# Performance work log

Hardware: AMD Instinct MI355X
Metric: run time of the kernel (lower is better)

## Reference

```python
import jax, jax.numpy as jnp
import numpy as np

N_HEAD = 16
CHUNK_SIZE = 64
TOP_B = 8
LOCAL_WINDOW = 256


def _l2_normalize(x, eps=1e-12):
    # matches torch F.normalize(dim=-1): x / max(||x||, eps)
    n = jnp.sqrt(jnp.sum(x * x, axis=-1, keepdims=True))
    return x / jnp.maximum(n, eps)


def setup_inputs() -> dict:
    key = jax.random.key(0)
    ks = jax.random.split(key, 9)
    B, T, C = 2, 2048, 1024
    s = lambda fan_in: 1.0 / np.sqrt(fan_in)
    return {
        "x": jax.random.normal(ks[0], (B, T, C), jnp.float32),
        "Wqkv": jax.random.normal(ks[1], (C, 3 * C), jnp.float32) * s(C),
        "bqkv": jax.random.normal(ks[2], (3 * C,), jnp.float32) * 0.02,
        "Wproj": jax.random.normal(ks[3], (C, C), jnp.float32) * s(C),
        "bproj": jax.random.normal(ks[4], (C,), jnp.float32) * 0.02,
        "Wrouter": jax.random.normal(ks[5], (C, 32), jnp.float32) * s(C),
        "brouter": jax.random.normal(ks[6], (32,), jnp.float32) * 0.02,
        "Wq_rt": jax.random.normal(ks[7], (C, 32), jnp.float32) * s(C),
        "bq_rt": jax.random.normal(ks[8], (32,), jnp.float32) * 0.02,
    }


def reference(x, Wqkv, bqkv, Wproj, bproj, Wrouter, brouter, Wq_rt, bq_rt):
    B, T, C = x.shape
    H = N_HEAD
    D = C // H

    # --- qkv projection ---
    qkv = x @ Wqkv + bqkv                       # [B,T,3C]
    q, k, v = jnp.split(qkv, 3, axis=-1)
    q = q.reshape(B, T, H, D).transpose(0, 2, 1, 3)  # [B,H,T,D]
    k = k.reshape(B, T, H, D).transpose(0, 2, 1, 3)
    v = v.reshape(B, T, H, D).transpose(0, 2, 1, 3)

    # --- routing (T > local_window + chunk_size) ---
    num_chunks = T // CHUNK_SIZE                 # T divisible -> no padding, mask all-True
    chunk_means = x.reshape(B, num_chunks, CHUNK_SIZE, C).mean(axis=2)  # [B,N,C]
    routing_embeds = chunk_means @ Wrouter + brouter                     # [B,N,32]
    q_rt = _l2_normalize(x @ Wq_rt + bq_rt)                              # [B,T,32]
    re_n = _l2_normalize(routing_embeds)
    routing_scores = jnp.einsum('btd,bnd->btn', q_rt, re_n)              # [B,T,N]
    _, chunk_indices = jax.lax.top_k(routing_scores, TOP_B)              # [B,T,top_b]

    # --- dense causal attention (forward path uses is_causal SDPA) ---
    scale = 1.0 / jnp.sqrt(jnp.asarray(D, x.dtype))
    scores = jnp.einsum('bhqd,bhkd->bhqk', q, k) * scale                 # [B,H,T,T]
    causal = jnp.tril(jnp.ones((T, T), dtype=bool))
    scores = jnp.where(causal[None, None], scores, -jnp.inf)
    attn = jax.nn.softmax(scores, axis=-1)
    y = jnp.einsum('bhqk,bhkd->bhqd', attn, v)                           # [B,H,T,D]
    y = y.transpose(0, 2, 1, 3).reshape(B, T, C)
    y = y @ Wproj + bproj

    return y, chunk_indices, routing_scores, routing_embeds
```

## Files before the change

kernel.cpp:

```cpp
#include <hip/hip_runtime.h>
#include <hip/hip_bf16.h>
#include <math.h>

#define B_   2
#define T_   2048
#define C_   1024
#define H_   16
#define D_   64
#define NCH  32
#define RD   32
#define TOPB 8

typedef __attribute__((ext_vector_type(8))) short bf16x8;
typedef __attribute__((ext_vector_type(4))) float f32x4;

static __device__ __forceinline__ unsigned short f2b(float f) {
    return __bfloat16_as_ushort(__float2bfloat16(f));
}

#define SCALE2 0.18033688f

__global__ __launch_bounds__(256) void prep_fused(
    const float* __restrict__ x, unsigned short* __restrict__ xb,
    const float* __restrict__ Wqkv, unsigned short* __restrict__ Wqt,
    const float* __restrict__ Wproj, unsigned short* __restrict__ Wpt,
    const float* __restrict__ Wq_rt, const float* __restrict__ bq_rt,
    float* __restrict__ qrt, float* __restrict__ cm)
{
    __shared__ float smem[64 * 65];
    const int bid = blockIdx.x;
    const int tid = threadIdx.x;

    if (bid < 2048) {
        const int i = bid * 256 + tid;
        float4 a = ((const float4*)x)[i * 2];
        float4 b = ((const float4*)x)[i * 2 + 1];
        bf16x8 o;
        o[0] = (short)f2b(a.x); o[1] = (short)f2b(a.y);
        o[2] = (short)f2b(a.z); o[3] = (short)f2b(a.w);
        o[4] = (short)f2b(b.x); o[5] = (short)f2b(b.y);
        o[6] = (short)f2b(b.z); o[7] = (short)f2b(b.w);
        *(bf16x8*)&xb[(size_t)i * 8] = o;
    } else if (bid < 3072) {
        const float* W; unsigned short* Wt; int N, local;
        if (bid < 2816) { W = Wqkv;  Wt = Wqt; N = 3072; local = bid - 2048; }
        else            { W = Wproj; Wt = Wpt; N = 1024; local = bid - 2816; }
        const int nblk = N >> 6;
        const int n0 = (local % nblk) * 64, k0 = (local / nblk) * 64;
        float (*t)[65] = (float(*)[65])smem;
#pragma unroll
        for (int i = 0; i < 4; i++) {
            const int f = tid + i * 256;
            const int r = f >> 4, c4 = (f & 15) * 4;
            float4 v = *(const float4*)&W[(size_t)(k0 + r) * N + n0 + c4];
            t[r][c4 + 0] = v.x; t[r][c4 + 1] = v.y;
            t[r][c4 + 2] = v.z; t[r][c4 + 3] = v.w;
        }
        __syncthreads();
#pragma unroll
        for (int i = 0; i < 2; i++) {
            const int s = tid + i * 256;
            const int rn = s >> 3, ck8 = (s & 7) * 8;
            bf16x8 o;
#pragma unroll
            for (int j = 0; j < 8; j++) o[j] = (short)f2b(t[ck8 + j][rn]);
            *(bf16x8*)&Wt[(size_t)(n0 + rn) * 1024 + k0 + ck8] = o;
        }
    } else if (bid < 4096) {
        float (*part)[4][32] = (float(*)[4][32])smem;
        const int r0 = (bid - 3072) * 4;
        const int g = tid >> 5;
        const int n = tid & 31;
        const float* w  = Wq_rt + (size_t)(g * 128) * RD + n;
        const float* a0 = x + (size_t)(r0 + 0) * C_ + g * 128;
        const float* a1 = x + (size_t)(r0 + 1) * C_ + g * 128;
        const float* a2 = x + (size_t)(r0 + 2) * C_ + g * 128;
        const float* a3 = x + (size_t)(r0 + 3) * C_ + g * 128;
        float acc0 = 0.f, acc1 = 0.f, acc2 = 0.f, acc3 = 0.f;
#pragma unroll 8
        for (int i = 0; i < 128; i += 4) {
            const float w0 = w[(i + 0) * RD];
            const float w1 = w[(i + 1) * RD];
            const float w2 = w[(i + 2) * RD];
            const float w3 = w[(i + 3) * RD];
            float4 x0 = *(const float4*)&a0[i];
            float4 x1 = *(const float4*)&a1[i];
            float4 x2 = *(const float4*)&a2[i];
            float4 x3 = *(const float4*)&a3[i];
            acc0 += x0.x * w0; acc0 += x0.y * w1; acc0 += x0.z * w2; acc0 += x0.w * w3;
            acc1 += x1.x * w0; acc1 += x1.y * w1; acc1 += x1.z * w2; acc1 += x1.w * w3;
            acc2 += x2.x * w0; acc2 += x2.y * w1; acc2 += x2.z * w2; acc2 += x2.w * w3;
            acc3 += x3.x * w0; acc3 += x3.y * w1; acc3 += x3.z * w2; acc3 += x3.w * w3;
        }
        part[g][0][n] = acc0;
        part[g][1][n] = acc1;
        part[g][2][n] = acc2;
        part[g][3][n] = acc3;
        __syncthreads();
        if (g < 4) {
            float s = part[0][g][n];
#pragma unroll
            for (int gg = 1; gg < 8; gg++) s += part[gg][g][n];
            s += bq_rt[n];
            float ss = s * s;
#pragma unroll
            for (int off = 16; off >= 1; off >>= 1) ss += __shfl_xor(ss, off, 32);
            qrt[(size_t)(r0 + g) * RD + n] = s / fmaxf(sqrtf(ss), 1e-12f);
        }
    } else {
        const int local = bid - 4096;
        const int bc = local & 63;
        const int b = bc >> 5, n = bc & 31;
        const int c = (local >> 6) * 256 + tid;
        const float* xp = x + ((size_t)b * T_ + n * 64) * C_;
        float s = 0.f;
        for (int i = 0; i < 64; i++) s += xp[(size_t)i * C_ + c];
        cm[(size_t)bc * C_ + c] = s * (1.0f / 64.0f);
    }
}

__global__ void embeds_kernel(const float* __restrict__ cm, const float* __restrict__ W,
                              const float* __restrict__ bias,
                              float* __restrict__ emb_out, float* __restrict__ ren)
{
    const int row  = blockIdx.x * 8 + (threadIdx.x >> 5);
    const int lane = threadIdx.x & 31;
    if (row >= B_ * NCH) return;
    const float* a = cm + (size_t)row * C_;
    float acc = 0.f;
    for (int k = 0; k < C_; k += 4) {
        float4 a4 = *(const float4*)&a[k];
        acc += a4.x * W[(k + 0) * RD + lane];
        acc += a4.y * W[(k + 1) * RD + lane];
        acc += a4.z * W[(k + 2) * RD + lane];
        acc += a4.w * W[(k + 3) * RD + lane];
    }
    acc += bias[lane];
    emb_out[(size_t)row * RD + lane] = acc;
    float ss = acc * acc;
#pragma unroll
    for (int off = 16; off >= 1; off >>= 1) ss += __shfl_xor(ss, off, 32);
    ren[(size_t)row * RD + lane] = acc / fmaxf(sqrtf(ss), 1e-12f);
}

__global__ __launch_bounds__(512, 4) void gemm_qkv_128x256(
    const unsigned short* __restrict__ A, const unsigned short* __restrict__ Bt,
    const float* __restrict__ bias,
    unsigned short* __restrict__ qp, unsigned short* __restrict__ kp,
    unsigned short* __restrict__ vp, int M, int N, int K)
{
    __shared__ unsigned short lds[3][12288];

    const int tid  = threadIdx.x;
    const int wid  = tid >> 6;
    const int lane = tid & 63;
    const int lr = lane & 15, lg = lane >> 4;
    const int wm = wid >> 2;
    const int wn = wid & 3;

    const int bid = blockIdx.x;
    const int swz = (bid & 7) * 48 + (bid >> 3);
    const int m0 = (swz & 31) << 7;
    const int n0 = (swz >> 5) << 8;

    const int srow = tid >> 2;
    const int sswz = (((srow & 3) ^ ((srow >> 2) & 3)) << 4);
    const int skel = (((tid & 3) << 4) ^ sswz) >> 1;
    const unsigned short* gA  = A  + (size_t)(m0 + srow) * K + skel;
    const unsigned short* gB0 = Bt + (size_t)(n0 + srow) * K + skel;
    const unsigned short* gB1 = Bt + (size_t)(n0 + srow + 128) * K + skel;
    const int lb = wid * 512;

#define QSTAGE(sl, kofs)                                                          \
    __builtin_amdgcn_global_load_lds(                                             \
        (const __attribute__((address_space(1))) int*)(gA + (kofs)),              \
        (__attribute__((address_space(3))) int*)&lds[sl][lb], 16, 0, 0);          \
    __builtin_amdgcn_global_load_lds(                                             \
        (const __attribute__((address_space(1))) int*)(gB0 + (kofs)),             \
        (__attribute__((address_space(3))) int*)&lds[sl][4096 + lb], 16, 0, 0);   \
    __builtin_amdgcn_global_load_lds(                                             \
        (const __attribute__((address_space(1))) int*)(gB1 + (kofs)),             \
        (__attribute__((address_space(3))) int*)&lds[sl][8192 + lb], 16, 0, 0);

    const int rswz = (((lr & 3) ^ ((lr >> 2) & 3)) << 4);
    const int acol = (((lg << 4) ^ rswz) >> 1);

    f32x4 acc[4][4];
#pragma unroll
    for (int i = 0; i < 4; i++)
#pragma unroll
        for (int j = 0; j < 4; j++) acc[i][j] = (f32x4){0.f, 0.f, 0.f, 0.f};

    const int nt = K >> 5;

    QSTAGE(0, 0)
    QSTAGE(1, 32)
    asm volatile("s_waitcnt vmcnt(3)" ::: "memory");
    __builtin_amdgcn_s_barrier();

    int cur = 0;
    for (int t = 0; t < nt; ++t) {
        int s2 = cur + 2; if (s2 >= 3) s2 -= 3;
        if (t + 2 < nt) { QSTAGE(s2, (t + 2) << 5) }

        const unsigned short* sA = &lds[cur][0];
        const unsigned short* sB = &lds[cur][4096];

        bf16x8 af[4], bfr[4];
#pragma unroll
        for (int mi = 0; mi < 4; mi++)
            af[mi] = *(const bf16x8*)&sA[(wm * 64 + mi * 16 + lr) * 32 + acol];
#pragma unroll
        for (int ni = 0; ni < 4; ni++)
            bfr[ni] = *(const bf16x8*)&sB[(wn * 64 + ni * 16 + lr) * 32 + acol];

        __builtin_amdgcn_s_setprio(1);
#pragma unroll
        for (int mi = 0; mi < 4; mi++)
#pragma unroll
            for (int ni = 0; ni < 4; ni++)
                acc[mi][ni] = __builtin_amdgcn_mfma_f32_16x16x32_bf16(
                    af[mi], bfr[ni], acc[mi][ni], 0, 0, 0);
        __builtin_amdgcn_s_setprio(0);

        if (t + 1 < nt) {
            if (t + 2 < nt) { asm volatile("s_waitcnt vmcnt(3)" ::: "memory"); }
            else            { asm volatile("s_waitcnt vmcnt(0)" ::: "memory"); }
            __builtin_amdgcn_s_barrier();
        }
        cur += 1; if (cur == 3) cur = 0;
    }
#undef QSTAGE

#pragma unroll
    for (int ni = 0; ni < 4; ni++) {
        const int col = n0 + wn * 64 + ni * 16 + lr;
        const float bv = bias[col];
        const int which = col >> 10;
        const int c  = col & 1023;
        const int hh = c >> 6;
        const int dd = c & 63;
        unsigned short* dst = (which == 0) ? qp : (which == 1) ? kp : vp;
        const float postmul = (which == 0) ? SCALE2 : 1.0f;
#pragma unroll
        for (int mi = 0; mi < 4; mi++) {
#pragma unroll
            for (int r = 0; r < 4; r++) {
                const int row = m0 + wm * 64 + mi * 16 + lg * 4 + r;
                const int bb = row >> 11, tt = row & 2047;
                dst[(((size_t)bb * H_ + hh) * T_ + tt) * D_ + dd] =
                    f2b((acc[mi][ni][r] + bv) * postmul);
            }
        }
    }
}

__global__ __launch_bounds__(256, 1) void gemm_proj_128(
    const unsigned short* __restrict__ A, const unsigned short* __restrict__ Bt,
    const float* __restrict__ bias, float* __restrict__ out, int M, int N, int K)
{
    __shared__ unsigned short lds[3][2][4096];

    const int tid  = threadIdx.x;
    const int lane = tid & 63;
    const int wave = tid >> 6;
    const int lr = lane & 15, lg = lane >> 4;
    const int wm = wave >> 1, wn = wave & 1;
    const int n0 = blockIdx.x * 128, m0 = blockIdx.y * 128;

    const int srow = tid >> 2;
    const int sswz = (((srow & 3) ^ ((srow >> 2) & 3)) << 4);
    const int skel = (((tid & 3) << 4) ^ sswz) >> 1;
    const unsigned short* gA0 = A  + (size_t)(m0 + srow) * K + skel;
    const unsigned short* gA1 = A  + (size_t)(m0 + srow + 64) * K + skel;
    const unsigned short* gB0 = Bt + (size_t)(n0 + srow) * K + skel;
    const unsigned short* gB1 = Bt + (size_t)(n0 + srow + 64) * K + skel;
    const int ldb = (tid & 0xC0) * 8;

#define PSTAGE(sl, kofs)                                                          \
    __builtin_amdgcn_global_load_lds(                                             \
        (const __attribute__((address_space(1))) int*)(gA0 + (kofs)),             \
        (__attribute__((address_space(3))) int*)&lds[sl][0][ldb], 16, 0, 0);      \
    __builtin_amdgcn_global_load_lds(                                             \
        (const __attribute__((address_space(1))) int*)(gA1 + (kofs)),             \
        (__attribute__((address_space(3))) int*)&lds[sl][0][2048 + ldb], 16, 0, 0); \
    __builtin_amdgcn_global_load_lds(                                             \
        (const __attribute__((address_space(1))) int*)(gB0 + (kofs)),             \
        (__attribute__((address_space(3))) int*)&lds[sl][1][ldb], 16, 0, 0);      \
    __builtin_amdgcn_global_load_lds(                                             \
        (const __attribute__((address_space(1))) int*)(gB1 + (kofs)),             \
        (__attribute__((address_space(3))) int*)&lds[sl][1][2048 + ldb], 16, 0, 0);

    const int rswz = (((lr & 3) ^ ((lr >> 2) & 3)) << 4);
    const int acol = (((lg << 4) ^ rswz) >> 1);

    f32x4 acc[4][4];
#pragma unroll
    for (int i = 0; i < 4; i++)
#pragma unroll
        for (int j = 0; j < 4; j++) acc[i][j] = (f32x4){0.f, 0.f, 0.f, 0.f};

    const int nt = K >> 5;

    PSTAGE(0, 0)
    PSTAGE(1, 32)
    asm volatile("s_waitcnt vmcnt(4)" ::: "memory");
    __builtin_amdgcn_s_barrier();

    int cur = 0;
    for (int t = 0; t < nt; ++t) {
        int s2 = cur + 2; if (s2 >= 3) s2 -= 3;
        if (t + 2 < nt) { PSTAGE(s2, (t + 2) << 5) }

        const unsigned short* sA = &lds[cur][0][0];
        const unsigned short* sB = &lds[cur][1][0];

        bf16x8 af[4], bfr[4];
#pragma unroll
        for (int mi = 0; mi < 4; mi++)
            af[mi] = *(const bf16x8*)&sA[(wm * 64 + mi * 16 + lr) * 32 + acol];
#pragma unroll
        for (int ni = 0; ni < 4; ni++)
            bfr[ni] = *(const bf16x8*)&sB[(wn * 64 + ni * 16 + lr) * 32 + acol];

        __builtin_amdgcn_s_setprio(1);
#pragma unroll
        for (int mi = 0; mi < 4; mi++)
#pragma unroll
            for (int ni = 0; ni < 4; ni++)
                acc[mi][ni] = __builtin_amdgcn_mfma_f32_16x16x32_bf16(
                    af[mi], bfr[ni], acc[mi][ni], 0, 0, 0);
        __builtin_amdgcn_s_setprio(0);

        if (t + 1 < nt) {
            if (t + 2 < nt) { asm volatile("s_waitcnt vmcnt(4)" ::: "memory"); }
            else            { asm volatile("s_waitcnt vmcnt(0)" ::: "memory"); }
            __builtin_amdgcn_s_barrier();
        }
        cur += 1; if (cur == 3) cur = 0;
    }
#undef PSTAGE

#pragma unroll
    for (int ni = 0; ni < 4; ni++) {
        const int col = n0 + wn * 64 + ni * 16 + lr;
        const float bv = bias[col];
#pragma unroll
        for (int mi = 0; mi < 4; mi++) {
#pragma unroll
            for (int r = 0; r < 4; r++) {
                const int row = m0 + wm * 64 + mi * 16 + lg * 4 + r;
                out[(size_t)row * N + col] = acc[mi][ni][r] + bv;
            }
        }
    }
}

__global__ void scores_topk(const float* __restrict__ qrt, const float* __restrict__ ren,
                            float* __restrict__ sc_out, float* __restrict__ idx_out)
{
    const int row = blockIdx.x * 64 + threadIdx.x;
    if (row >= B_ * T_) return;
    const int b = row / T_;
    float q[RD];
#pragma unroll
    for (int i = 0; i < RD; i++) q[i] = qrt[(size_t)row * RD + i];
    const float* rb = ren + (size_t)b * NCH * RD;
    float s[NCH];
#pragma unroll 4
    for (int n = 0; n < NCH; n++) {
        float acc = 0.f;
#pragma unroll
        for (int i = 0; i < RD; i++) acc += q[i] * rb[n * RD + i];
        s[n] = acc;
        sc_out[(size_t)row * NCH + n] = acc;
    }
    unsigned mask = 0;
    for (int t = 0; t < TOPB; t++) {
        float best = -INFINITY;
        int bi = 0;
#pragma unroll
        for (int n = 0; n < NCH; n++) {
            const bool ok = !((mask >> n) & 1u) && (s[n] > best);
            if (ok) { best = s[n]; bi = n; }
        }
        mask |= (1u << bi);
        idx_out[(size_t)row * TOPB + t] = (float)bi;
    }
}

#define SW(row, idx) ((idx) ^ (((row) & 7) << 3))

__global__ __launch_bounds__(256) void attn_mfma(
    const unsigned short* __restrict__ qg, const unsigned short* __restrict__ kg,
    const unsigned short* __restrict__ vg, unsigned short* __restrict__ y)
{
    const int bid = blockIdx.x;
    const int xcd = bid & 7;
    const int h   = xcd + 8 * ((bid >> 3) & 1);
    const int b   = (bid >> 4) & 1;
    const int i   = bid >> 5;
    const int qt  = (i & 8) ? ((i & 16) ? (i - 24) : (i + 8)) : (31 - i);

    const int tid  = threadIdx.x;
    const int wave = tid >> 6;
    const int lane = tid & 63;
    const int lg = lane >> 4;
    const int lr = lane & 15;

    __shared__ short Ks[2][64 * 64];
    __shared__ short Vt[2][64 * 64];

    const size_t base = ((size_t)(b * H_ + h) * T_) * D_;

    bf16x8 qf0, qf1;
    {
        const short* qp = (const short*)qg + base + (size_t)(qt * 64 + wave * 16 + lr) * D_;
        qf0 = *(const bf16x8*)&qp[lg * 8];
        qf1 = *(const bf16x8*)&qp[32 + lg * 8];
    }

    const int srr = tid >> 2;
    const int sc0 = (tid & 3) * 16;
    const int vrp = tid & 31;
    const int vcg = tid >> 5;
    const int kv0   = 2 * vrp;
    const int vslot = ((kv0 >> 5) << 5) + (((kv0 >> 2) & 3) << 3) +
                      (((kv0 >> 4) & 1) << 2) + (kv0 & 3);

    const int kst0 = SW(srr, srr * 64 + sc0);
    const int kst1 = SW(srr, srr * 64 + sc0 + 8);
    const int rsw = (lr & 7) << 3;

    bf16x8 kreg0, kreg1, vreg0, vreg1;

    float m_run = -INFINITY, l_run = 0.f;
    f32x4 oacc[4];
#pragma unroll
    for (int r = 0; r < 4; r++) oacc[r] = (f32x4){0.f, 0.f, 0.f, 0.f};
    const int qrow_g = qt * 64 + wave * 16 + lr;

#define VPACK(buf)                                                              \
    {                                                                           \
        const unsigned* v0d = (const unsigned*)&vreg0;                          \
        const unsigned* v1d = (const unsigned*)&vreg1;                          \
        _Pragma("unroll")                                                       \
        for (int jj = 0; jj < 8; jj++) {                                        \
            const unsigned sel = (jj & 1) ? 0x07060302u : 0x05040100u;          \
            const unsigned dw = __builtin_amdgcn_perm(v1d[jj >> 1], v0d[jj >> 1], sel); \
            *(unsigned*)&Vt[buf][SW(jj, (vcg * 8 + jj) * 64 + vslot)] = dw;     \
        }                                                                       \
    }

    const short* kpn = (const short*)kg + base + (size_t)srr * D_ + sc0;
    const short* vpn = (const short*)vg + base + (size_t)kv0 * D_ + vcg * 8;

    kreg0 = *(const bf16x8*)kpn;
    kreg1 = *(const bf16x8*)(kpn + 8);
    vreg0 = *(const bf16x8*)vpn;
    vreg1 = *(const bf16x8*)(vpn + D_);
    kpn += 4096; vpn += 4096;

    *(bf16x8*)&Ks[0][kst0] = kreg0;
    *(bf16x8*)&Ks[0][kst1] = kreg1;
    VPACK(0)

    if (qt >= 1) {
        kreg0 = *(const bf16x8*)kpn;
        kreg1 = *(const bf16x8*)(kpn + 8);
        vreg0 = *(const bf16x8*)vpn;
        vreg1 = *(const bf16x8*)(vpn + D_);
        kpn += 4096; vpn += 4096;
    }
    __syncthreads();

    for (int kt = 0; kt <= qt; ++kt) {
        const int cur = kt & 1;

        if (kt < qt) {
            *(bf16x8*)&Ks[cur ^ 1][kst0] = kreg0;
            *(bf16x8*)&Ks[cur ^ 1][kst1] = kreg1;
            VPACK(cur ^ 1)
        }
        if (kt + 2 <= qt) {
            kreg0 = *(const bf16x8*)kpn;
            kreg1 = *(const bf16x8*)(kpn + 8);
            vreg0 = *(const bf16x8*)vpn;
            vreg1 = *(const bf16x8*)(vpn + D_);
            kpn += 4096; vpn += 4096;
        }

        f32x4 s[4];
        __builtin_amdgcn_s_setprio(1);
#pragma unroll
        for (int cb = 0; cb < 4; cb++) {
            const int row = cb * 16 + lr;
            bf16x8 kf0 = *(const bf16x8*)&Ks[cur][(row * 64 + lg * 8) ^ rsw];
            bf16x8 kf1 = *(const bf16x8*)&Ks[cur][(row * 64 + 32 + lg * 8) ^ rsw];
            f32x4 acc = (f32x4){0.f, 0.f, 0.f, 0.f};
            acc = __builtin_amdgcn_mfma_f32_16x16x32_bf16(kf0, qf0, acc, 0, 0, 0);
            acc = __builtin_amdgcn_mfma_f32_16x16x32_bf16(kf1, qf1, acc, 0, 0, 0);
            s[cb] = acc;
        }
        __builtin_amdgcn_s_setprio(0);

        if (kt == qt) {
#pragma unroll
            for (int cb = 0; cb < 4; cb++)
#pragma unroll
                for (int r = 0; r < 4; r++)
                    if (kt * 64 + cb * 16 + lg * 4 + r > qrow_g) s[cb][r] = -INFINITY;
        }

        float rm;
        {
            const float t0 = fmaxf(fmaxf(s[0][0], s[0][1]), fmaxf(s[0][2], s[0][3]));
            const float t1 = fmaxf(fmaxf(s[1][0], s[1][1]), fmaxf(s[1][2], s[1][3]));
            const float t2 = fmaxf(fmaxf(s[2][0], s[2][1]), fmaxf(s[2][2], s[2][3]));
            const float t3 = fmaxf(fmaxf(s[3][0], s[3][1]), fmaxf(s[3][2], s[3][3]));
            rm = fmaxf(fmaxf(t0, t1), fmaxf(t2, t3));
        }
        rm = fmaxf(rm, __shfl_xor(rm, 16));
        rm = fmaxf(rm, __shfl_xor(rm, 32));

        if (!__all(rm <= m_run + 8.0f)) {
            const float mnew = fmaxf(m_run, rm);
            const float fsc  = exp2f(m_run - mnew);
            m_run = mnew;
            l_run *= fsc;
            float fr[4];
#pragma unroll
            for (int r = 0; r < 4; r++) fr[r] = __shfl(fsc, lg * 4 + r);
#pragma unroll
            for (int db = 0; db < 4; db++)
#pragma unroll
                for (int r = 0; r < 4; r++) oacc[db][r] *= fr[r];
        }

        float p[4][4];
#pragma unroll
        for (int cb = 0; cb < 4; cb++)
#pragma unroll
            for (int r = 0; r < 4; r++)
                p[cb][r] = exp2f(s[cb][r] - m_run);
        float rs;
        {
            const float t0 = (p[0][0] + p[0][1]) + (p[0][2] + p[0][3]);
            const float t1 = (p[1][0] + p[1][1]) + (p[1][2] + p[1][3]);
            const float t2 = (p[2][0] + p[2][1]) + (p[2][2] + p[2][3]);
            const float t3 = (p[3][0] + p[3][1]) + (p[3][2] + p[3][3]);
            rs = (t0 + t1) + (t2 + t3);
        }
        rs += __shfl_xor(rs, 16);
        rs += __shfl_xor(rs, 32);
        l_run += rs;

        bf16x8 pf0, pf1;
#pragma unroll
        for (int r = 0; r < 4; r++) {
            pf0[r]     = (short)f2b(p[0][r]);
            pf0[4 + r] = (short)f2b(p[1][r]);
            pf1[r]     = (short)f2b(p[2][r]);
            pf1[4 + r] = (short)f2b(p[3][r]);
        }

        __builtin_amdgcn_s_setprio(1);
#pragma unroll
        for (int db = 0; db < 4; db++) {
            const int row = db * 16 + lr;
            bf16x8 vf0 = *(const bf16x8*)&Vt[cur][(row * 64 + lg * 8) ^ rsw];
            bf16x8 vf1 = *(const bf16x8*)&Vt[cur][(row * 64 + 32 + lg * 8) ^ rsw];
            oacc[db] = __builtin_amdgcn_mfma_f32_16x16x32_bf16(pf0, vf0, oacc[db], 0, 0, 0);
            oacc[db] = __builtin_amdgcn_mfma_f32_16x16x32_bf16(pf1, vf1, oacc[db], 0, 0, 0);
        }
        __builtin_amdgcn_s_setprio(0);

        __syncthreads();
    }
#undef VPACK

#pragma unroll
    for (int r = 0; r < 4; r++) {
        const float lrow = __shfl(l_run, lg * 4 + r);
        const float inv = 1.0f / lrow;
        const int trow = qt * 64 + wave * 16 + lg * 4 + r;
        unsigned short* yp = y + (size_t)(b * T_ + trow) * C_ + h * D_;
#pragma unroll
        for (int db = 0; db < 4; db++)
            yp[db * 16 + lr] = f2b(oacc[db][r] * inv);
    }
}

extern "C" void kernel_launch(void* const* d_in, const int* in_sizes, int n_in,
                              void* d_out, int out_size, void* d_ws, size_t ws_size,
                              hipStream_t stream)
{
    const float* x       = (const float*)d_in[0];
    const float* Wqkv    = (const float*)d_in[1];
    const float* bqkv    = (const float*)d_in[2];
    const float* Wproj   = (const float*)d_in[3];
    const float* bproj   = (const float*)d_in[4];
    const float* Wrouter = (const float*)d_in[5];
    const float* brouter = (const float*)d_in[6];
    const float* Wq_rt   = (const float*)d_in[7];
    const float* bq_rt   = (const float*)d_in[8];

    float* out = (float*)d_out;
    char*  ws  = (char*)d_ws;

    const size_t MT  = (size_t)B_ * T_;
    const size_t QKV = MT * C_;

    unsigned short* xb   = (unsigned short*)ws;
    unsigned short* Wqt  = xb  + QKV;
    unsigned short* Wpt  = Wqt + (size_t)3 * C_ * C_;
    unsigned short* q    = Wpt + (size_t)C_ * C_;
    unsigned short* k    = q + QKV;
    unsigned short* v    = k + QKV;
    unsigned short* yab  = v + QKV;
    float* cm   = (float*)(yab + QKV);
    float* qrt  = cm  + (size_t)B_ * NCH * C_;
    float* ren  = qrt + MT * RD;

    float* y_out   = out;
    float* idx_out = out + QKV;
    float* sc_out  = idx_out + MT * TOPB;
    float* emb_out = sc_out + MT * NCH;

    prep_fused<<<4352, 256, 0, stream>>>(x, xb, Wqkv, Wqt, Wproj, Wpt,
                                         Wq_rt, bq_rt, qrt, cm);

    gemm_qkv_128x256<<<dim3(384), 512, 0, stream>>>(
        xb, Wqt, bqkv, q, k, v, (int)MT, 3 * C_, C_);

    embeds_kernel<<<8, 256, 0, stream>>>(cm, Wrouter, brouter, emb_out, ren);
    scores_topk<<<(int)(MT / 64), 64, 0, stream>>>(qrt, ren, sc_out, idx_out);

    attn_mfma<<<dim3(1024), 256, 0, stream>>>(q, k, v, yab);

    gemm_proj_128<<<dim3(C_ / 128, MT / 128), 256, 0, stream>>>(
        yab, Wpt, bproj, y_out, (int)MT, C_, C_);
}
```

Measured before the change: 178.8 us.

## Use 128-row query tiles with 8 waves sharing each K/V tile

The attention kernel now handles 128 query rows per block with 512 threads (8 waves), so each K/V tile staged in shared memory serves twice as many queries. The grid halves to 512 blocks, the per-thread staging load shrinks to match, and the causal mask applies to the last two key tiles. This is meant to halve the K/V global loads and LDS staging per query, at the cost of fewer blocks, coarser causal load balance, and diagonal work on waves whose rows are fully masked in the final tile.

```diff
diff --git a/kernel.cpp b/kernel.cpp
--- a/kernel.cpp
+++ b/kernel.cpp
@@ -391,7 +391,7 @@
 
 #define SW(row, idx) ((idx) ^ (((row) & 7) << 3))
 
-__global__ __launch_bounds__(256) void attn_mfma(
+__global__ __launch_bounds__(512) void attn_mfma(
     const unsigned short* __restrict__ qg, const unsigned short* __restrict__ kg,
     const unsigned short* __restrict__ vg, unsigned short* __restrict__ y)
 {
@@ -400,7 +400,7 @@
     const int h   = xcd + 8 * ((bid >> 3) & 1);
     const int b   = (bid >> 4) & 1;
     const int i   = bid >> 5;
-    const int qt  = (i & 8) ? ((i & 16) ? (i - 24) : (i + 8)) : (31 - i);
+    const int qt  = (i < 8) ? (15 - i) : (i - 8);
 
     const int tid  = threadIdx.x;
     const int wave = tid >> 6;
@@ -415,78 +415,75 @@
 
     bf16x8 qf0, qf1;
     {
-        const short* qp = (const short*)qg + base + (size_t)(qt * 64 + wave * 16 + lr) * D_;
+        const short* qp = (const short*)qg + base + (size_t)(qt * 128 + wave * 16 + lr) * D_;
         qf0 = *(const bf16x8*)&qp[lg * 8];
         qf1 = *(const bf16x8*)&qp[32 + lg * 8];
     }
 
-    const int srr = tid >> 2;
-    const int sc0 = (tid & 3) * 16;
+    const int srr = tid >> 3;
+    const int sc0 = (tid & 7) * 8;
     const int vrp = tid & 31;
     const int vcg = tid >> 5;
     const int kv0   = 2 * vrp;
     const int vslot = ((kv0 >> 5) << 5) + (((kv0 >> 2) & 3) << 3) +
                       (((kv0 >> 4) & 1) << 2) + (kv0 & 3);
 
-    const int kst0 = SW(srr, srr * 64 + sc0);
-    const int kst1 = SW(srr, srr * 64 + sc0 + 8);
+    const int kst = SW(srr, srr * 64 + sc0);
     const int rsw = (lr & 7) << 3;
 
-    bf16x8 kreg0, kreg1, vreg0, vreg1;
+    bf16x8 kreg;
+    uint2 va, vb;
 
     float m_run = -INFINITY, l_run = 0.f;
     f32x4 oacc[4];
 #pragma unroll
     for (int r = 0; r < 4; r++) oacc[r] = (f32x4){0.f, 0.f, 0.f, 0.f};
-    const int qrow_g = qt * 64 + wave * 16 + lr;
+    const int qrow_g = qt * 128 + wave * 16 + lr;
 
 #define VPACK(buf)                                                              \
     {                                                                           \
-        const unsigned* v0d = (const unsigned*)&vreg0;                          \
-        const unsigned* v1d = (const unsigned*)&vreg1;                          \
-        _Pragma("unroll")                                                       \
-        for (int jj = 0; jj < 8; jj++) {                                        \
-            const unsigned sel = (jj & 1) ? 0x07060302u : 0x05040100u;          \
-            const unsigned dw = __builtin_amdgcn_perm(v1d[jj >> 1], v0d[jj >> 1], sel); \
-            *(unsigned*)&Vt[buf][SW(jj, (vcg * 8 + jj) * 64 + vslot)] = dw;     \
-        }                                                                       \
+        const unsigned d0 = __builtin_amdgcn_perm(vb.x, va.x, 0x05040100u);     \
+        const unsigned d1 = __builtin_amdgcn_perm(vb.x, va.x, 0x07060302u);     \
+        const unsigned d2 = __builtin_amdgcn_perm(vb.y, va.y, 0x05040100u);     \
+        const unsigned d3 = __builtin_amdgcn_perm(vb.y, va.y, 0x07060302u);     \
+        const int dr = vcg * 4;                                                 \
+        *(unsigned*)&Vt[buf][SW(dr + 0, (dr + 0) * 64 + vslot)] = d0;           \
+        *(unsigned*)&Vt[buf][SW(dr + 1, (dr + 1) * 64 + vslot)] = d1;           \
+        *(unsigned*)&Vt[buf][SW(dr + 2, (dr + 2) * 64 + vslot)] = d2;           \
+        *(unsigned*)&Vt[buf][SW(dr + 3, (dr + 3) * 64 + vslot)] = d3;           \
     }
 
     const short* kpn = (const short*)kg + base + (size_t)srr * D_ + sc0;
-    const short* vpn = (const short*)vg + base + (size_t)kv0 * D_ + vcg * 8;
-
-    kreg0 = *(const bf16x8*)kpn;
-    kreg1 = *(const bf16x8*)(kpn + 8);
-    vreg0 = *(const bf16x8*)vpn;
-    vreg1 = *(const bf16x8*)(vpn + D_);
+    const short* vpn = (const short*)vg + base + (size_t)kv0 * D_ + vcg * 4;
+
+    kreg = *(const bf16x8*)kpn;
+    va   = *(const uint2*)vpn;
+    vb   = *(const uint2*)(vpn + D_);
     kpn += 4096; vpn += 4096;
 
-    *(bf16x8*)&Ks[0][kst0] = kreg0;
-    *(bf16x8*)&Ks[0][kst1] = kreg1;
+    *(bf16x8*)&Ks[0][kst] = kreg;
     VPACK(0)
 
-    if (qt >= 1) {
-        kreg0 = *(const bf16x8*)kpn;
-        kreg1 = *(const bf16x8*)(kpn + 8);
-        vreg0 = *(const bf16x8*)vpn;
-        vreg1 = *(const bf16x8*)(vpn + D_);
+    const int nkt = 2 * qt + 2;
+    if (nkt > 1) {
+        kreg = *(const bf16x8*)kpn;
+        va   = *(const uint2*)vpn;
+        vb   = *(const uint2*)(vpn + D_);
         kpn += 4096; vpn += 4096;
     }
     __syncthreads();
 
-    for (int kt = 0; kt <= qt; ++kt) {
+    for (int kt = 0; kt < nkt; ++kt) {
         const int cur = kt & 1;
 
-        if (kt < qt) {
-            *(bf16x8*)&Ks[cur ^ 1][kst0] = kreg0;
-            *(bf16x8*)&Ks[cur ^ 1][kst1] = kreg1;
+        if (kt + 1 < nkt) {
+            *(bf16x8*)&Ks[cur ^ 1][kst] = kreg;
             VPACK(cur ^ 1)
         }
-        if (kt + 2 <= qt) {
-            kreg0 = *(const bf16x8*)kpn;
-            kreg1 = *(const bf16x8*)(kpn + 8);
-            vreg0 = *(const bf16x8*)vpn;
-            vreg1 = *(const bf16x8*)(vpn + D_);
+        if (kt + 2 < nkt) {
+            kreg = *(const bf16x8*)kpn;
+            va   = *(const uint2*)vpn;
+            vb   = *(const uint2*)(vpn + D_);
             kpn += 4096; vpn += 4096;
         }
 
@@ -504,7 +501,7 @@
         }
         __builtin_amdgcn_s_setprio(0);
 
-        if (kt == qt) {
+        if (kt >= 2 * qt) {
 #pragma unroll
             for (int cb = 0; cb < 4; cb++)
 #pragma unroll
@@ -583,7 +580,7 @@
     for (int r = 0; r < 4; r++) {
         const float lrow = __shfl(l_run, lg * 4 + r);
         const float inv = 1.0f / lrow;
-        const int trow = qt * 64 + wave * 16 + lg * 4 + r;
+        const int trow = qt * 128 + wave * 16 + lg * 4 + r;
         unsigned short* yp = y + (size_t)(b * T_ + trow) * C_ + h * D_;
 #pragma unroll
         for (int db = 0; db < 4; db++)
@@ -636,7 +633,7 @@
     embeds_kernel<<<8, 256, 0, stream>>>(cm, Wrouter, brouter, emb_out, ren);
     scores_topk<<<(int)(MT / 64), 64, 0, stream>>>(qrt, ren, sc_out, idx_out);
 
-    attn_mfma<<<dim3(1024), 256, 0, stream>>>(q, k, v, yab);
+    attn_mfma<<<dim3(512), 512, 0, stream>>>(q, k, v, yab);
 
     gemm_proj_128<<<dim3(C_ / 128, MT / 128), 256, 0, stream>>>(
         yab, Wpt, bproj, y_out, (int)MT, C_, C_);
```

Measured after the change: 184.2 us. 3.0% more time.

## Split causal attention KV range into two halves and merge with combine kernel

Applied to the files above, without the earlier changes.

Each query tile's causal KV range is now split into two halves processed by separate blocks, doubling the grid. Each block writes an unnormalized partial output in bf16 plus per-row (max, sum) statistics. A new combine kernel rescales and merges the two partials and writes the normalized result in the layout the projection GEMM expects. The aim is more parallelism and less tail imbalance across long causal rows, at the cost of an extra launch, extra global traffic for the partial outputs, and bf16 rounding of the unnormalized partials.

```diff
diff --git a/kernel.cpp b/kernel.cpp
--- a/kernel.cpp
+++ b/kernel.cpp
@@ -16,6 +16,9 @@
 
 static __device__ __forceinline__ unsigned short f2b(float f) {
     return __bfloat16_as_ushort(__float2bfloat16(f));
+}
+static __device__ __forceinline__ float b2f(unsigned short u) {
+    union { unsigned u32; float f; } c; c.u32 = ((unsigned)u) << 16; return c.f;
 }
 
 #define SCALE2 0.18033688f
@@ -393,14 +396,18 @@
 
 __global__ __launch_bounds__(256) void attn_mfma(
     const unsigned short* __restrict__ qg, const unsigned short* __restrict__ kg,
-    const unsigned short* __restrict__ vg, unsigned short* __restrict__ y)
+    const unsigned short* __restrict__ vg,
+    unsigned short* __restrict__ Op0, unsigned short* __restrict__ Op1,
+    float2* __restrict__ mlbuf)
 {
-    const int bid = blockIdx.x;
-    const int xcd = bid & 7;
-    const int h   = xcd + 8 * ((bid >> 3) & 1);
-    const int b   = (bid >> 4) & 1;
-    const int i   = bid >> 5;
-    const int qt  = (i & 8) ? ((i & 16) ? (i - 24) : (i + 8)) : (31 - i);
+    const int bid  = blockIdx.x;
+    const int xcd  = bid & 7;
+    const int h    = xcd + 8 * ((bid >> 3) & 1);
+    const int b    = (bid >> 4) & 1;
+    const int rest = bid >> 5;
+    const int half = rest & 1;
+    const int i    = rest >> 1;
+    const int qt   = 31 - i;
 
     const int tid  = threadIdx.x;
     const int wave = tid >> 6;
@@ -408,10 +415,28 @@
     const int lg = lane >> 4;
     const int lr = lane & 15;
 
+    const int bh = b * H_ + h;
+
+    const int ntt = qt + 1;
+    const int nh0 = (ntt + 1) >> 1;
+    const int kts = half ? nh0 : 0;
+    const int kte = half ? ntt : nh0;
+
+    float m_run = -INFINITY, l_run = 0.f;
+
+    if (kts >= kte) {
+        if (lg == 0 && wave < 4) {
+            const int trow = qt * 64 + wave * 16 + lr;
+            mlbuf[(size_t)half * (B_ * H_ * T_) + (size_t)bh * T_ + trow] =
+                make_float2(-INFINITY, 0.f);
+        }
+        return;
+    }
+
     __shared__ short Ks[2][64 * 64];
     __shared__ short Vt[2][64 * 64];
 
-    const size_t base = ((size_t)(b * H_ + h) * T_) * D_;
+    const size_t base = ((size_t)bh * T_) * D_;
 
     bf16x8 qf0, qf1;
     {
@@ -434,7 +459,6 @@
 
     bf16x8 kreg0, kreg1, vreg0, vreg1;
 
-    float m_run = -INFINITY, l_run = 0.f;
     f32x4 oacc[4];
 #pragma unroll
     for (int r = 0; r < 4; r++) oacc[r] = (f32x4){0.f, 0.f, 0.f, 0.f};
@@ -452,8 +476,8 @@
         }                                                                       \
     }
 
-    const short* kpn = (const short*)kg + base + (size_t)srr * D_ + sc0;
-    const short* vpn = (const short*)vg + base + (size_t)kv0 * D_ + vcg * 8;
+    const short* kpn = (const short*)kg + base + (size_t)(kts * 64 + srr) * D_ + sc0;
+    const short* vpn = (const short*)vg + base + (size_t)(kts * 64 + kv0) * D_ + vcg * 8;
 
     kreg0 = *(const bf16x8*)kpn;
     kreg1 = *(const bf16x8*)(kpn + 8);
@@ -465,7 +489,7 @@
     *(bf16x8*)&Ks[0][kst1] = kreg1;
     VPACK(0)
 
-    if (qt >= 1) {
+    if (kts + 1 < kte) {
         kreg0 = *(const bf16x8*)kpn;
         kreg1 = *(const bf16x8*)(kpn + 8);
         vreg0 = *(const bf16x8*)vpn;
@@ -474,15 +498,15 @@
     }
     __syncthreads();
 
-    for (int kt = 0; kt <= qt; ++kt) {
-        const int cur = kt & 1;
-
-        if (kt < qt) {
+    for (int kt = kts; kt < kte; ++kt) {
+        const int cur = (kt - kts) & 1;
+
+        if (kt + 1 < kte) {
             *(bf16x8*)&Ks[cur ^ 1][kst0] = kreg0;
             *(bf16x8*)&Ks[cur ^ 1][kst1] = kreg1;
             VPACK(cur ^ 1)
         }
-        if (kt + 2 <= qt) {
+        if (kt + 2 < kte) {
             kreg0 = *(const bf16x8*)kpn;
             kreg1 = *(const bf16x8*)(kpn + 8);
             vreg0 = *(const bf16x8*)vpn;
@@ -579,16 +603,49 @@
     }
 #undef VPACK
 
+    unsigned short* Op = half ? Op1 : Op0;
 #pragma unroll
     for (int r = 0; r < 4; r++) {
-        const float lrow = __shfl(l_run, lg * 4 + r);
-        const float inv = 1.0f / lrow;
         const int trow = qt * 64 + wave * 16 + lg * 4 + r;
-        unsigned short* yp = y + (size_t)(b * T_ + trow) * C_ + h * D_;
+        unsigned short* op = Op + ((size_t)bh * T_ + trow) * D_;
 #pragma unroll
         for (int db = 0; db < 4; db++)
-            yp[db * 16 + lr] = f2b(oacc[db][r] * inv);
-    }
+            op[db * 16 + lr] = f2b(oacc[db][r]);
+    }
+    if (lg == 0) {
+        const int trow = qt * 64 + wave * 16 + lr;
+        mlbuf[(size_t)half * (B_ * H_ * T_) + (size_t)bh * T_ + trow] =
+            make_float2(m_run, l_run);
+    }
+}
+
+__global__ __launch_bounds__(256) void combine_kernel(
+    const unsigned short* __restrict__ Op0, const unsigned short* __restrict__ Op1,
+    const float2* __restrict__ mlbuf, unsigned short* __restrict__ y)
+{
+    const int ro = blockIdx.x * 16 + (threadIdx.x >> 4);
+    const int d0 = (threadIdx.x & 15) * 4;
+
+    const float2 ml0 = mlbuf[ro];
+    const float2 ml1 = mlbuf[B_ * H_ * T_ + ro];
+    const float m  = fmaxf(ml0.x, ml1.x);
+    const float w0 = exp2f(ml0.x - m);
+    const float w1 = exp2f(ml1.x - m);
+    const float inv = 1.0f / (ml0.y * w0 + ml1.y * w1);
+
+    const size_t off = (size_t)ro * D_ + d0;
+    const ushort4 o0 = *(const ushort4*)&Op0[off];
+    const ushort4 o1 = *(const ushort4*)&Op1[off];
+
+    ushort4 res;
+    res.x = f2b((b2f(o0.x) * w0 + b2f(o1.x) * w1) * inv);
+    res.y = f2b((b2f(o0.y) * w0 + b2f(o1.y) * w1) * inv);
+    res.z = f2b((b2f(o0.z) * w0 + b2f(o1.z) * w1) * inv);
+    res.w = f2b((b2f(o0.w) * w0 + b2f(o1.w) * w1) * inv);
+
+    const int bh = ro >> 11, t = ro & 2047;
+    const int b = bh >> 4, h = bh & 15;
+    *(ushort4*)&y[((size_t)(b * T_ + t) * C_) + h * D_ + d0] = res;
 }
 
 extern "C" void kernel_launch(void* const* d_in, const int* in_sizes, int n_in,
@@ -621,6 +678,9 @@
     float* cm   = (float*)(yab + QKV);
     float* qrt  = cm  + (size_t)B_ * NCH * C_;
     float* ren  = qrt + MT * RD;
+    float2* mlbuf = (float2*)(ren + (size_t)B_ * NCH * RD);
+    unsigned short* Op1 = (unsigned short*)(mlbuf + 2 * B_ * H_ * T_);
+    unsigned short* Op0 = xb;
 
     float* y_out   = out;
     float* idx_out = out + QKV;
@@ -636,7 +696,8 @@
     embeds_kernel<<<8, 256, 0, stream>>>(cm, Wrouter, brouter, emb_out, ren);
     scores_topk<<<(int)(MT / 64), 64, 0, stream>>>(qrt, ren, sc_out, idx_out);
 
-    attn_mfma<<<dim3(1024), 256, 0, stream>>>(q, k, v, yab);
+    attn_mfma<<<dim3(2048), 256, 0, stream>>>(q, k, v, Op0, Op1, mlbuf);
+    combine_kernel<<<dim3(4096), 256, 0, stream>>>(Op0, Op1, mlbuf, yab);
 
     gemm_proj_128<<<dim3(C_ / 128, MT / 128), 256, 0, stream>>>(
         yab, Wpt, bproj, y_out, (int)MT, C_, C_);
```

New measurement: 177.2 us, median of 2. No clear change (-0.9%).
